# Performance work log

Measured on AMD Instinct MI355X. Metric: run time of the kernel, lower is better.

## Reference

```python
import jax, jax.numpy as jnp
import numpy as np

N_NODES = 100000
THETA = jnp.asarray([0.2, -0.4, 0.3, -0.15, 0.05], dtype=jnp.float32)


def setup_inputs() -> dict:
    key = jax.random.key(0)
    k1, k2, k3, k4 = jax.random.split(key, 4)
    n_edges = 1600000
    feat = jax.random.normal(k1, (N_NODES, 32), dtype=jnp.float32)
    src = jax.random.randint(k2, (n_edges,), 0, N_NODES, dtype=jnp.int32)
    dst = jax.random.randint(k3, (n_edges,), 0, N_NODES, dtype=jnp.int32)
    mask = jax.random.uniform(k4, (n_edges,), dtype=jnp.float32)
    return {"feat": feat, "src": src, "dst": dst, "mask": mask}


def reference(feat, src, dst, mask):
    # degree = sum of edge mask into destination nodes (copy_e + sum)
    deg = jax.ops.segment_sum(mask, dst, num_segments=N_NODES)
    # D^{-1/2} with clamp(min=1)
    d_invsqrt = jnp.power(jnp.maximum(deg, 1.0), -0.5)[:, None]  # [N,1]

    h = THETA[0] * feat
    for k in range(1, THETA.shape[0]):
        # unnormalized Laplacian step: feat - D^{-1/2} A D^{-1/2} feat
        scaled = feat * d_invsqrt                      # [N,d]
        msg = scaled[src] * mask[:, None]              # [E,d] gather + edge scale
        agg = jax.ops.segment_sum(msg, dst, num_segments=N_NODES)  # [N,d]
        feat = feat - agg * d_invsqrt
        h = h + THETA[k] * feat
    return h
```

## Files before the change

kernel.cpp:

```cpp
#include <hip/hip_runtime.h>
#include <hip/hip_fp16.h>


#define FDIM 32
#define DLO_BITS 8
#define BKT_NODES 256
#define S_FIX 1536
#define MAXBKT 512


__global__ __launch_bounds__(512) void p3_kernel(const int* __restrict__ src,
                                                 const int* __restrict__ dst,
                                                 const float* __restrict__ mask,
                                                 int* __restrict__ lofsT,
                                                 int2* __restrict__ esp,
                                                 int NBLKp, int nbkt, int E) {
    __shared__ int sdst[S_FIX];
    __shared__ int ssrc[S_FIX];
    __shared__ float smask[S_FIX];
    __shared__ int lh[MAXBKT];
    __shared__ int ws[8];
    int b = blockIdx.x;
    int tid = threadIdx.x;
    int e0 = b * S_FIX;
    int n = E - e0;
    if (n > S_FIX) n = S_FIX;
    if (n < 0) n = 0;
    for (int t = tid; t < n; t += 512) {
        sdst[t] = dst[e0 + t];
        ssrc[t] = src[e0 + t];
        smask[t] = mask[e0 + t];
    }
    lh[tid] = 0;
    __syncthreads();
    for (int t = tid; t < n; t += 512) atomicAdd(&lh[sdst[t] >> DLO_BITS], 1);
    __syncthreads();
    int v = lh[tid];
    int lane = tid & 63, wv = tid >> 6;
    int x = v;
#pragma unroll
    for (int o = 1; o < 64; o <<= 1) {
        int y = __shfl_up(x, o);
        if (lane >= o) x += y;
    }
    if (lane == 63) ws[wv] = x;
    __syncthreads();
    int add = 0;
    for (int i = 0; i < wv; ++i) add += ws[i];
    x += add;
    int excl = x - v;
    lh[tid] = excl;
    if (tid < nbkt) lofsT[(size_t)tid * NBLKp + b] = excl;
    if (tid == 0) lofsT[(size_t)nbkt * NBLKp + b] = n;
    __syncthreads();
    for (int t = tid; t < n; t += 512) {
        int d = sdst[t];
        int g = d >> DLO_BITS;
        int pos = e0 + atomicAdd(&lh[g], 1);
        int2 vv;
        vv.x = ssrc[t] | ((d & (BKT_NODES - 1)) << 17);
        vv.y = __float_as_int(smask[t]);
        esp[pos] = vv;
    }
}

__global__ void scanR_kernel(const int* __restrict__ lofsT, int* __restrict__ R, int NBLKp) {
    int g = blockIdx.x;
    int tid = threadIdx.x;
    int s = 0;
    for (int t = tid; t < NBLKp; t += 256) s += lofsT[(size_t)g * NBLKp + t];
#pragma unroll
    for (int o = 1; o < 64; o <<= 1) s += __shfl_xor(s, o);
    __shared__ int wsum[4];
    int lane = tid & 63, wv = tid >> 6;
    if (lane == 0) wsum[wv] = s;
    __syncthreads();
    if (tid == 0) R[g] = wsum[0] + wsum[1] + wsum[2] + wsum[3];
}

__global__ __launch_bounds__(512) void p4_kernel(const int2* __restrict__ esp,
                                                 const int* __restrict__ lofsT,
                                                 const int* __restrict__ R,
                                                 int* __restrict__ esI,
                                                 int* __restrict__ row_ptr,
                                                 float* __restrict__ dinv,
                                                 const float4* __restrict__ feat,
                                                 uint2* __restrict__ m0,
                                                 int NBLKp, int nbkt, int N, int E) {
    __shared__ int lcnt[BKT_NODES];
    __shared__ int lofs[BKT_NODES];
    __shared__ float ldeg[BKT_NODES];
    __shared__ int ws[8];
    int g = blockIdx.x;
    int tid = threadIdx.x;
    if (tid < BKT_NODES) { lcnt[tid] = 0; ldeg[tid] = 0.0f; }
    __syncthreads();
    int segbase = R[g];
    for (int b = tid; b < NBLKp; b += 512) {
        int st = lofsT[(size_t)g * NBLKp + b];
        int en = lofsT[(size_t)(g + 1) * NBLKp + b];
        int base = b * S_FIX;
        for (int i = st; i < en; ++i) {
            int2 v = esp[base + i];
            int dlo = v.x >> 17;
            atomicAdd(&lcnt[dlo], 1);
            atomicAdd(&ldeg[dlo], __int_as_float(v.y));
        }
    }
    __syncthreads();
    int v = (tid < BKT_NODES) ? lcnt[tid] : 0;
    int lane = tid & 63, wv = tid >> 6;
    int x = v;
#pragma unroll
    for (int o = 1; o < 64; o <<= 1) {
        int y = __shfl_up(x, o);
        if (lane >= o) x += y;
    }
    if (lane == 63) ws[wv] = x;
    __syncthreads();
    int add = 0;
    for (int i = 0; i < wv; ++i) add += ws[i];
    x += add;
    int excl = x - v;
    if (tid < BKT_NODES) {
        lofs[tid] = excl;
        int node = g * BKT_NODES + tid;
        if (node < N) {
            row_ptr[node] = segbase + excl;
            float d = ldeg[tid];
            d = d > 1.0f ? d : 1.0f;
            float di = 1.0f / sqrtf(d);
            dinv[node] = di;
            ldeg[tid] = di;
        }
    }
    if (g == 0 && tid == 0) row_ptr[N] = E;
    __syncthreads();
    if (tid < BKT_NODES) lcnt[tid] = 0;
    __syncthreads();
    for (int b = tid; b < NBLKp; b += 512) {
        int st = lofsT[(size_t)g * NBLKp + b];
        int en = lofsT[(size_t)(g + 1) * NBLKp + b];
        int base = b * S_FIX;
        for (int i = st; i < en; ++i) {
            int2 v2 = esp[base + i];
            int dlo = v2.x >> 17;
            int r = atomicAdd(&lcnt[dlo], 1);
            float mk = __int_as_float(v2.y);
            int wq = (int)(mk * 32768.0f + 0.5f);
            if (wq > 32767) wq = 32767;
            esI[segbase + lofs[dlo] + r] = (v2.x & 0x1FFFF) | (wq << 17);
        }
    }
    int base_node = g * BKT_NODES;
    for (int t = tid; t < BKT_NODES * 8; t += 512) {
        int nl = t >> 3;
        int n2 = base_node + nl;
        if (n2 >= N) break;
        float di = ldeg[nl];
        float4 f = feat[(size_t)n2 * 8 + (t & 7)];
        __half2 a = __float22half2_rn(make_float2(f.x * di, f.y * di));
        __half2 bb = __float22half2_rn(make_float2(f.z * di, f.w * di));
        uint2 m;
        m.x = *(unsigned*)&a;
        m.y = *(unsigned*)&bb;
        m0[(size_t)n2 * 8 + (t & 7)] = m;
    }
}

template <int MODE>
__global__ __launch_bounds__(256) void aggregate_kernel(
    const float4* __restrict__ fown, float4* __restrict__ fwr,
    const uint2* __restrict__ gin, uint2* __restrict__ gout,
    float4* __restrict__ out,
    const int* __restrict__ row_ptr, const int* __restrict__ es,
    const float* __restrict__ dinv, float theta, float theta0, int N) {
    int wave = (blockIdx.x * blockDim.x + threadIdx.x) >> 6;
    int lane = threadIdx.x & 63;
    int node = wave * 4 + (lane >> 4);
    if (node >= N) return;
    int l16 = lane & 15;
    int c = l16 & 7;
    int q = l16 >> 3;
    int b = row_ptr[node];
    int e = row_ptr[node + 1];
    float ax = 0.f, ay = 0.f, az = 0.f, aw = 0.f;
    float bx = 0.f, by = 0.f, bz = 0.f, bw = 0.f;
    int i = b + q;
    for (; i + 2 < e; i += 4) {
        int e0 = es[i];
        int e1 = es[i + 2];
        float w0 = (float)((unsigned)e0 >> 17) * (1.0f / 32768.0f);
        float w1 = (float)((unsigned)e1 >> 17) * (1.0f / 32768.0f);
        uint2 r0 = gin[(size_t)(e0 & 0x1FFFF) * 8 + c];
        uint2 r1 = gin[(size_t)(e1 & 0x1FFFF) * 8 + c];
        float2 p0 = __half22float2(*(const __half2*)&r0.x);
        float2 p1 = __half22float2(*(const __half2*)&r0.y);
        float2 p2 = __half22float2(*(const __half2*)&r1.x);
        float2 p3 = __half22float2(*(const __half2*)&r1.y);
        ax += w0 * p0.x; ay += w0 * p0.y; az += w0 * p1.x; aw += w0 * p1.y;
        bx += w1 * p2.x; by += w1 * p2.y; bz += w1 * p3.x; bw += w1 * p3.y;
    }
    if (i < e) {
        int e0 = es[i];
        float w0 = (float)((unsigned)e0 >> 17) * (1.0f / 32768.0f);
        uint2 r0 = gin[(size_t)(e0 & 0x1FFFF) * 8 + c];
        float2 p0 = __half22float2(*(const __half2*)&r0.x);
        float2 p1 = __half22float2(*(const __half2*)&r0.y);
        ax += w0 * p0.x; ay += w0 * p0.y; az += w0 * p1.x; aw += w0 * p1.y;
    }
    ax += bx; ay += by; az += bz; aw += bw;
    ax += __shfl_xor(ax, 8);
    ay += __shfl_xor(ay, 8);
    az += __shfl_xor(az, 8);
    aw += __shfl_xor(aw, 8);
    float4 fav = fown[(size_t)node * 8 + c];
    float di = dinv[node];
    float fx = fav.x - ax * di;
    float fy = fav.y - ay * di;
    float fz = fav.z - az * di;
    float fw = fav.w - aw * di;
    if (MODE != 2) {
        if (q == 0) {
            float4 t; t.x = fx; t.y = fy; t.z = fz; t.w = fw;
            fwr[(size_t)node * 8 + c] = t;
            __half2 a = __float22half2_rn(make_float2(fx * di, fy * di));
            __half2 bb = __float22half2_rn(make_float2(fz * di, fw * di));
            uint2 m;
            m.x = *(unsigned*)&a;
            m.y = *(unsigned*)&bb;
            gout[(size_t)node * 8 + c] = m;
        } else {
            float4 o;
            if (MODE == 1) {
                o.x = theta0 * fav.x + theta * fx;
                o.y = theta0 * fav.y + theta * fy;
                o.z = theta0 * fav.z + theta * fz;
                o.w = theta0 * fav.w + theta * fw;
            } else {
                o = out[(size_t)node * 8 + c];
                o.x += theta * fx; o.y += theta * fy;
                o.z += theta * fz; o.w += theta * fw;
            }
            out[(size_t)node * 8 + c] = o;
        }
    } else {
        if (q == 1) {
            float4 o = out[(size_t)node * 8 + c];
            o.x += theta * fx; o.y += theta * fy;
            o.z += theta * fz; o.w += theta * fw;
            out[(size_t)node * 8 + c] = o;
        }
    }
}


__global__ void fb_deg_kernel(const int* __restrict__ dst, const float* __restrict__ mask,
                              float* __restrict__ deg, int E) {
    int e = blockIdx.x * blockDim.x + threadIdx.x;
    if (e < E) atomicAdd(&deg[dst[e]], mask[e]);
}

__global__ void fb_dinv_kernel(float* __restrict__ deg, int N) {
    int i = blockIdx.x * blockDim.x + threadIdx.x;
    if (i < N) {
        float d = deg[i];
        d = d > 1.0f ? d : 1.0f;
        deg[i] = 1.0f / sqrtf(d);
    }
}

__global__ void fb_init_kernel(const float4* __restrict__ feat, float4* __restrict__ fbuf,
                               float4* __restrict__ out, int n4) {
    int i = blockIdx.x * blockDim.x + threadIdx.x;
    if (i < n4) {
        float4 f = feat[i];
        fbuf[i] = f;
        float4 o;
        o.x = 0.2f * f.x; o.y = 0.2f * f.y; o.z = 0.2f * f.z; o.w = 0.2f * f.w;
        out[i] = o;
    }
}

__global__ void fb_scatter_kernel(const float4* __restrict__ fbuf, const float* __restrict__ dinv,
                                  const int* __restrict__ src, const int* __restrict__ dst,
                                  const float* __restrict__ mask, float* __restrict__ agg, int E) {
    int t = blockIdx.x * blockDim.x + threadIdx.x;
    int e = t >> 3;
    if (e >= E) return;
    int c4 = t & 7;
    int s = src[e];
    int d = dst[e];
    float w = mask[e] * dinv[s];
    float4 f = fbuf[s * 8 + c4];
    float* ap = agg + (size_t)d * FDIM + c4 * 4;
    atomicAdd(ap + 0, f.x * w);
    atomicAdd(ap + 1, f.y * w);
    atomicAdd(ap + 2, f.z * w);
    atomicAdd(ap + 3, f.w * w);
}

__global__ void fb_update_kernel(float4* __restrict__ fbuf, float4* __restrict__ agg,
                                 const float* __restrict__ dinv, float4* __restrict__ out,
                                 float theta, int n4) {
    int t = blockIdx.x * blockDim.x + threadIdx.x;
    if (t >= n4) return;
    int node = t >> 3;
    float di = dinv[node];
    float4 a = agg[t];
    float4 z; z.x = 0.f; z.y = 0.f; z.z = 0.f; z.w = 0.f;
    agg[t] = z;
    float4 f = fbuf[t];
    f.x -= a.x * di; f.y -= a.y * di; f.z -= a.z * di; f.w -= a.w * di;
    fbuf[t] = f;
    float4 o = out[t];
    o.x += theta * f.x; o.y += theta * f.y; o.z += theta * f.z; o.w += theta * f.w;
    out[t] = o;
}


static inline size_t align_up(size_t x) { return (x + 63) & ~(size_t)63; }

extern "C" void kernel_launch(void* const* d_in, const int* in_sizes, int n_in,
                              void* d_out, int out_size, void* d_ws, size_t ws_size,
                              hipStream_t stream) {
    const float* feat = (const float*)d_in[0];
    const int* src = (const int*)d_in[1];
    const int* dst = (const int*)d_in[2];
    const float* mask = (const float*)d_in[3];
    float* out = (float*)d_out;

    const int N = in_sizes[0] / FDIM;
    const int E = in_sizes[1];
    const float thetas[5] = {0.2f, -0.4f, 0.3f, -0.15f, 0.05f};
    const int B = 256;

    const int nbkt = (N + BKT_NODES - 1) / BKT_NODES;
    const int NBLKp = (E + S_FIX - 1) / S_FIX;

    size_t o_dinv = 0;
    size_t o_rp    = align_up(o_dinv + N);
    size_t o_esI   = align_up(o_rp + N + 1);
    size_t o_m0    = align_up(o_esI + (size_t)E);
    size_t o_m1    = align_up(o_m0 + (size_t)N * 16);
    size_t o_esp   = align_up(o_m1 + (size_t)N * 16);
    size_t o_lofsT = align_up(o_esp + 2 * (size_t)E);
    size_t o_R     = align_up(o_lofsT + (size_t)(nbkt + 1) * NBLKp);
    size_t o_f     = align_up(o_R + nbkt + 1);
    size_t need = (o_f + (size_t)N * FDIM) * 4;

    float* wsf = (float*)d_ws;
    int* wsi = (int*)d_ws;

    int nbE = (E + B - 1) / B;
    int nbN = (N + B - 1) / B;

    if (ws_size >= need && N <= (1 << 17) && nbkt <= MAXBKT) {
        float* dinv = wsf + o_dinv;
        int* row_ptr = wsi + o_rp;
        int* esI = wsi + o_esI;
        uint2* m0 = (uint2*)(wsi + o_m0);
        uint2* m1 = (uint2*)(wsi + o_m1);
        int2* esp = (int2*)(wsi + o_esp);
        int* lofsT = wsi + o_lofsT;
        int* R = wsi + o_R;
        float4* f = (float4*)(wsf + o_f);

        p3_kernel<<<NBLKp, 512, 0, stream>>>(src, dst, mask, lofsT, esp, NBLKp, nbkt, E);
        scanR_kernel<<<nbkt + 1, 256, 0, stream>>>(lofsT, R, NBLKp);
        p4_kernel<<<nbkt, 512, 0, stream>>>(esp, lofsT, R, esI, row_ptr, dinv,
                                            (const float4*)feat, m0, NBLKp, nbkt, N, E);

        int aggWaves = (N + 3) / 4;
        int agg_blocks = (aggWaves * 64 + B - 1) / B;
        aggregate_kernel<1><<<agg_blocks, B, 0, stream>>>((const float4*)feat, f, m0, m1,
                                                          (float4*)out, row_ptr, esI, dinv,
                                                          thetas[1], thetas[0], N);
        aggregate_kernel<0><<<agg_blocks, B, 0, stream>>>(f, f, m1, m0, (float4*)out,
                                                          row_ptr, esI, dinv, thetas[2], 0.f, N);
        aggregate_kernel<0><<<agg_blocks, B, 0, stream>>>(f, f, m0, m1, (float4*)out,
                                                          row_ptr, esI, dinv, thetas[3], 0.f, N);
        aggregate_kernel<2><<<agg_blocks, B, 0, stream>>>(f, f, m1, m0, (float4*)out,
                                                          row_ptr, esI, dinv, thetas[4], 0.f, N);
    } else {
        float* deg = wsf;
        float* agg = deg + align_up(N);
        float* fbuf = agg + (size_t)N * FDIM;

        hipMemsetAsync(d_ws, 0, (align_up(N) + (size_t)N * FDIM) * 4, stream);
        fb_deg_kernel<<<nbE, B, 0, stream>>>(dst, mask, deg, E);
        fb_dinv_kernel<<<nbN, B, 0, stream>>>(deg, N);

        int n4 = N * (FDIM / 4);
        fb_init_kernel<<<(n4 + B - 1) / B, B, 0, stream>>>((const float4*)feat, (float4*)fbuf,
                                                           (float4*)out, n4);
        long long sc_threads = (long long)E * 8;
        int sc_blocks = (int)((sc_threads + B - 1) / B);
        for (int k = 1; k < 5; ++k) {
            fb_scatter_kernel<<<sc_blocks, B, 0, stream>>>((const float4*)fbuf, deg, src, dst,
                                                           mask, agg, E);
            fb_update_kernel<<<(n4 + B - 1) / B, B, 0, stream>>>((float4*)fbuf, (float4*)agg,
                                                                 deg, (float4*)out, thetas[k], n4);
        }
    }
}
```

Measured before the change: 193.3 us.

## Stage bucket edges in LDS and parallelize per-block edge loops in p4

p4 now prefix-sums the per-source-block edge counts of its bucket, copies the bucket's edges into shared memory during the degree pass, and reuses that staged copy in the scatter pass, so esp is not read from global memory a second time. The per-block inner loops also spread across 4 lanes instead of one thread walking each block serially. The cost is about 60KB of LDS per block, which lowers occupancy, plus extra scan and sync steps. A global-memory fallback path is kept for buckets that overflow the staging buffer.

```diff
diff --git a/kernel.cpp b/kernel.cpp
--- a/kernel.cpp
+++ b/kernel.cpp
@@ -7,6 +7,8 @@
 #define BKT_NODES 256
 #define S_FIX 1536
 #define MAXBKT 512
+#define MAXNBLK 2048
+#define PCAP 5120
 
 
 __global__ __launch_bounds__(512) void p3_kernel(const int* __restrict__ src,
@@ -87,29 +89,60 @@
                                                  const float4* __restrict__ feat,
                                                  uint2* __restrict__ m0,
                                                  int NBLKp, int nbkt, int N, int E) {
+    __shared__ int2 sstage[PCAP];
+    __shared__ int pseg[MAXNBLK];
     __shared__ int lcnt[BKT_NODES];
     __shared__ int lofs[BKT_NODES];
     __shared__ float ldeg[BKT_NODES];
     __shared__ int ws[8];
+    __shared__ int carry;
     int g = blockIdx.x;
     int tid = threadIdx.x;
+    int lane = tid & 63, wv = tid >> 6;
     if (tid < BKT_NODES) { lcnt[tid] = 0; ldeg[tid] = 0.0f; }
+    if (tid == 0) carry = 0;
     __syncthreads();
     int segbase = R[g];
-    for (int b = tid; b < NBLKp; b += 512) {
+    for (int base = 0; base < NBLKp; base += 512) {
+        int b = base + tid;
+        int c = 0;
+        if (b < NBLKp)
+            c = lofsT[(size_t)(g + 1) * NBLKp + b] - lofsT[(size_t)g * NBLKp + b];
+        int x = c;
+#pragma unroll
+        for (int o = 1; o < 64; o <<= 1) {
+            int y = __shfl_up(x, o);
+            if (lane >= o) x += y;
+        }
+        if (lane == 63) ws[wv] = x;
+        __syncthreads();
+        int add = 0;
+        for (int i = 0; i < wv; ++i) add += ws[i];
+        x += add;
+        int cc = carry;
+        if (b < NBLKp) pseg[b] = x - c + cc;
+        __syncthreads();
+        if (tid == 511) carry = cc + x;
+        __syncthreads();
+    }
+    int T = carry;
+    bool staged = (T <= PCAP);
+    int grp = tid >> 2, l4 = tid & 3;
+    for (int b = grp; b < NBLKp; b += 128) {
         int st = lofsT[(size_t)g * NBLKp + b];
         int en = lofsT[(size_t)(g + 1) * NBLKp + b];
         int base = b * S_FIX;
-        for (int i = st; i < en; ++i) {
+        int pb = pseg[b];
+        for (int i = st + l4; i < en; i += 4) {
             int2 v = esp[base + i];
             int dlo = v.x >> 17;
             atomicAdd(&lcnt[dlo], 1);
             atomicAdd(&ldeg[dlo], __int_as_float(v.y));
+            if (staged) sstage[pb + (i - st)] = v;
         }
     }
     __syncthreads();
     int v = (tid < BKT_NODES) ? lcnt[tid] : 0;
-    int lane = tid & 63, wv = tid >> 6;
     int x = v;
 #pragma unroll
     for (int o = 1; o < 64; o <<= 1) {
@@ -138,18 +171,30 @@
     __syncthreads();
     if (tid < BKT_NODES) lcnt[tid] = 0;
     __syncthreads();
-    for (int b = tid; b < NBLKp; b += 512) {
-        int st = lofsT[(size_t)g * NBLKp + b];
-        int en = lofsT[(size_t)(g + 1) * NBLKp + b];
-        int base = b * S_FIX;
-        for (int i = st; i < en; ++i) {
-            int2 v2 = esp[base + i];
+    if (staged) {
+        for (int k = tid; k < T; k += 512) {
+            int2 v2 = sstage[k];
             int dlo = v2.x >> 17;
             int r = atomicAdd(&lcnt[dlo], 1);
             float mk = __int_as_float(v2.y);
             int wq = (int)(mk * 32768.0f + 0.5f);
             if (wq > 32767) wq = 32767;
             esI[segbase + lofs[dlo] + r] = (v2.x & 0x1FFFF) | (wq << 17);
+        }
+    } else {
+        for (int b = grp; b < NBLKp; b += 128) {
+            int st = lofsT[(size_t)g * NBLKp + b];
+            int en = lofsT[(size_t)(g + 1) * NBLKp + b];
+            int base = b * S_FIX;
+            for (int i = st + l4; i < en; i += 4) {
+                int2 v2 = esp[base + i];
+                int dlo = v2.x >> 17;
+                int r = atomicAdd(&lcnt[dlo], 1);
+                float mk = __int_as_float(v2.y);
+                int wq = (int)(mk * 32768.0f + 0.5f);
+                if (wq > 32767) wq = 32767;
+                esI[segbase + lofs[dlo] + r] = (v2.x & 0x1FFFF) | (wq << 17);
+            }
         }
     }
     int base_node = g * BKT_NODES;
@@ -355,7 +400,7 @@
     int nbE = (E + B - 1) / B;
     int nbN = (N + B - 1) / B;
 
-    if (ws_size >= need && N <= (1 << 17) && nbkt <= MAXBKT) {
+    if (ws_size >= need && N <= (1 << 17) && nbkt <= MAXBKT && NBLKp <= MAXNBLK) {
         float* dinv = wsf + o_dinv;
         int* row_ptr = wsi + o_rp;
         int* esI = wsi + o_esI;
```

Result: faster. 174.9 us (-9.5%).
